# Performance work log

Measured on AMD Instinct MI355X. Metric: run time of the kernel, lower is better.

Reference implementation:

```python
import jax, jax.numpy as jnp
import numpy as np

B, T, IN, H, N, W, R, NW, OUT = 16, 64, 256, 512, 256, 64, 4, 1, 256
NM = 1 + 2 * NW  # read modes
EPS = 1e-6

# interface slice offsets
_sizes = [R*W, R, NW*W, NW, NW*W, NW*W, R, NW, NW, R*NM]
_offs = np.concatenate([[0], np.cumsum(_sizes)])

def _oneplus(x):
    return 1.0 + jax.nn.softplus(x)

def _content_weights(M, keys, strengths):
    # M: [B,N,W], keys: [B,h,W], strengths: [B,h] -> [B,h,N]
    Mn = M / (jnp.linalg.norm(M, axis=-1, keepdims=True) + EPS)
    kn = keys / (jnp.linalg.norm(keys, axis=-1, keepdims=True) + EPS)
    sim = jnp.einsum('bnw,bhw->bhn', Mn, kn)
    return jax.nn.softmax(_oneplus(strengths)[..., None] * sim, axis=-1)

def setup_inputs() -> dict:
    key = jax.random.key(0)
    ks = jax.random.split(key, 5)
    s = 0.02
    return {
        'inputs': jax.random.normal(ks[0], (T, B, IN), jnp.float32),
        'W_ih': jax.random.normal(ks[1], (4*H, IN + R*W), jnp.float32) * s,
        'W_hh': jax.random.normal(ks[2], (4*H, H), jnp.float32) * s,
        'b_ih': jnp.zeros((4*H,), jnp.float32),
        'b_hh': jnp.zeros((4*H,), jnp.float32),
        'W_int': jax.random.normal(ks[3], (H, int(_offs[-1])), jnp.float32) * s,
        'b_int': jnp.zeros((int(_offs[-1]),), jnp.float32),
        'W_out': jax.random.normal(ks[4], (OUT, H + R*W), jnp.float32) * s,
        'b_out': jnp.zeros((OUT,), jnp.float32),
    }

def _dnc_forward(inputs, W_ih, W_hh, b_ih, b_hh, W_int, b_int, W_out, b_out):
    off_diag = 1.0 - jnp.eye(N, dtype=inputs.dtype)

    def step(carry, x_t):
        h, c, M, usage, link, prec, wr, ww_prev, read_words = carry
        ctrl_in = jnp.concatenate([x_t, read_words.reshape(B, -1)], axis=1)
        gates = ctrl_in @ W_ih.T + h @ W_hh.T + (b_ih + b_hh)
        i, f, g, o = jnp.split(gates, 4, axis=1)  # torch LSTM gate order
        c = jax.nn.sigmoid(f) * c + jax.nn.sigmoid(i) * jnp.tanh(g)
        h = jax.nn.sigmoid(o) * jnp.tanh(c)

        itf = h @ W_int + b_int
        def sl(j, shape):
            return itf[:, _offs[j]:_offs[j+1]].reshape((B,) + shape)
        read_keys = sl(0, (R, W)); read_str = sl(1, (R,))
        write_keys = sl(2, (NW, W)); write_str = sl(3, (NW,))
        erase = jax.nn.sigmoid(sl(4, (NW, W)))
        write_vec = jax.nn.sigmoid(sl(5, (NW, W)))
        free_gate = jax.nn.sigmoid(sl(6, (R,)))
        alloc_gate = jax.nn.sigmoid(sl(7, (NW,)))
        write_gate = jax.nn.sigmoid(sl(8, (NW,)))
        modes = jax.nn.softmax(sl(9, (R, NM)), axis=2)

        # usage with previous write weights and free gates over previous reads
        psi = jnp.prod(1.0 - free_gate[:, :, None] * wr, axis=1)  # [B,N]
        ww_agg = 1.0 - jnp.prod(1.0 - ww_prev, axis=1)
        usage = (usage + ww_agg - usage * ww_agg) * psi

        # allocation weighting (sort ascending usage)
        idx = jnp.argsort(usage, axis=1)
        u_s = jnp.take_along_axis(usage, idx, axis=1)
        prod_excl = jnp.cumprod(jnp.concatenate([jnp.ones((B, 1), usage.dtype), u_s[:, :-1]], axis=1), axis=1)
        a_s = (1.0 - u_s) * prod_excl
        alloc = jnp.zeros_like(usage).at[jnp.arange(B)[:, None], idx].set(a_s)

        cw = _content_weights(M, write_keys, write_str)  # [B,NW,N]
        ww = write_gate[..., None] * (alloc_gate[..., None] * alloc[:, None, :] + (1.0 - alloc_gate[..., None]) * cw)

        # memory erase + write
        M = M * jnp.prod(1.0 - ww[:, :, :, None] * erase[:, :, None, :], axis=1)
        M = M + jnp.einsum('bhn,bhw->bnw', ww, write_vec)

        # temporal link update (uses old precedence)
        ww_i = ww[..., :, None]; ww_j = ww[..., None, :]
        link = (1.0 - ww_i - ww_j) * link + ww_i * prec[:, :, None, :]
        link = link * off_diag
        prec = (1.0 - ww.sum(-1, keepdims=True)) * prec + ww

        fwd = jnp.einsum('bwij,brj->brwi', link, wr)
        bwd = jnp.einsum('bwji,brj->brwi', link, wr)
        cr = _content_weights(M, read_keys, read_str)  # [B,R,N]
        mb, mf, mc = modes[..., :NW], modes[..., NW:2*NW], modes[..., 2*NW]
        wr = jnp.einsum('brw,brwn->brn', mb, bwd) + jnp.einsum('brw,brwn->brn', mf, fwd) + mc[..., None] * cr
        read_words = jnp.einsum('brn,bnw->brw', wr, M)

        pre = jnp.concatenate([h, read_words.reshape(B, -1)], axis=1)
        out = pre @ W_out.T + b_out
        return (h, c, M, usage, link, prec, wr, ww, read_words), out

    z = jnp.zeros
    dt = inputs.dtype
    carry0 = (z((B, H), dt), z((B, H), dt), z((B, N, W), dt), z((B, N), dt),
              z((B, NW, N, N), dt), z((B, NW, N), dt), z((B, R, N), dt),
              z((B, NW, N), dt), z((B, R, W), dt))
    _, outs = jax.lax.scan(step, carry0, inputs)
    return outs  # [T,B,OUT]

def reference(inputs, W_ih, W_hh, b_ih, b_hh, W_int, b_int, W_out, b_out):
    return _dnc_forward(inputs, W_ih, W_hh, b_ih, b_hh, W_int, b_int, W_out, b_out)
```

## Files before the change

### kernel.cpp

```cpp
#include <hip/hip_runtime.h>
#include <math.h>

#define BT 256
#define GRID 144

#define Bx 16
#define Tt 64
#define INx 256

__device__ __forceinline__ float sigm(float v) { return 1.0f / (1.0f + expf(-v)); }
__device__ __forceinline__ float oneplusf(float v) { return 1.0f + ((v > 15.0f) ? v : log1pf(expf(v))); }
__device__ __forceinline__ float4 ld4(const float* p) { return *reinterpret_cast<const float4*>(p); }

#define SCOPE_A __HIP_MEMORY_SCOPE_AGENT
__device__ __forceinline__ float gld(const float* p) {
    return __hip_atomic_load(p, __ATOMIC_RELAXED, SCOPE_A);
}
__device__ __forceinline__ void gst(float* p, float v) {
    __hip_atomic_store(p, v, __ATOMIC_RELAXED, SCOPE_A);
}
__device__ __forceinline__ float2 gld2(const float* p) {
    union { unsigned long long u; float2 f; } c;
    c.u = __hip_atomic_load(reinterpret_cast<const unsigned long long*>(p), __ATOMIC_RELAXED, SCOPE_A);
    return c.f;
}
__device__ __forceinline__ unsigned gldU(const unsigned* p) {
    return __hip_atomic_load(p, __ATOMIC_RELAXED, SCOPE_A);
}
__device__ __forceinline__ void gstU(unsigned* p, unsigned v) {
    __hip_atomic_store(p, v, __ATOMIC_RELAXED, SCOPE_A);
}

__device__ unsigned int g_flags[GRID];
__device__ unsigned int g_gen = 0;

__device__ __forceinline__ void gsync(unsigned tgt) {
    asm volatile("" ::: "memory");
    __builtin_amdgcn_s_waitcnt(0);
    __syncthreads();
    const int tid = threadIdx.x;
    if (blockIdx.x == 0) {
        if (tid < GRID) {
            if (tid == 0) gstU(&g_flags[0], tgt);
            while (gldU(&g_flags[tid]) < tgt) __builtin_amdgcn_s_sleep(1);
        }
        __syncthreads();
        if (tid == 0) gstU(&g_gen, tgt);
    } else {
        if (tid == 0) {
            gstU(&g_flags[blockIdx.x], tgt);
            while (gldU(&g_gen) < tgt) __builtin_amdgcn_s_sleep(1);
        }
        __syncthreads();
    }
    asm volatile("" ::: "memory");
}

#define ZERO_FLOATS 1376256

__global__ __launch_bounds__(BT)
void k_dnc(const float* __restrict__ x,
           const float* __restrict__ W_ih, const float* __restrict__ W_hh,
           const float* __restrict__ b_ih, const float* __restrict__ b_hh,
           const float* __restrict__ W_int, const float* __restrict__ b_int,
           const float* __restrict__ W_out, const float* __restrict__ b_out,
           float* __restrict__ outp, float* __restrict__ ws)
{
    const int bl = blockIdx.x, tid = threadIdx.x;

    float* h0   = ws;
    float* h1   = ws + 8192;
    float* cst  = ws + 16384;
    float* Mb   = ws + 24576;
    float* usg  = ws + 286720;
    float* lnk  = ws + 290816;
    float* pr0  = ws + 1339392;
    float* pr1  = ws + 1343488;
    float* wrb  = ws + 1347584;
    float* wwb  = ws + 1363968;
    float* rwb  = ws + 1368064;
    float* nrm  = ws + 1372160;
    float* itf  = ws + 1376256;
    float* ers  = ws + 1383792;
    float* wvs  = ws + 1384816;
    float* rso  = ws + 1385840;
    float* mds  = ws + 1385904;
    float* oh   = ws + 1386096;
    float* bwdb = ws + 1402480;
    float* fwdb = ws + 1418864;

    __shared__ float smem[4096];
    __shared__ int s_idx[256];
    __shared__ unsigned s_base;

    if (tid == 0) s_base = gldU(&g_gen);
    __syncthreads();
    unsigned bseq = s_base;

    for (int i = bl * BT + tid; i < ZERO_FLOATS; i += GRID * BT) gst(ws + i, 0.0f);
    gsync(++bseq);

    for (int t = 0; t < Tt; ++t) {
        const float* hr = (t & 1) ? h1 : h0;
        float*       hw = (t & 1) ? h0 : h1;
        const float* pr_r = (t & 1) ? pr1 : pr0;
        float*       pr_w = (t & 1) ? pr0 : pr1;

        if (bl < 128) {
            float* red = smem;
            int pl = tid >> 2, ks = tid & 3;
            int p = bl * 64 + pl;
            int b = p & 15, j = p >> 4;
            float a0 = 0, a1 = 0, a2 = 0, a3 = 0;
            const float *w0, *w1, *w2, *w3;
            int kofs = (ks < 2) ? ks * 256 : (ks - 2) * 256;
            if (ks < 2) {
                w0 = W_ih + (j)        * 512 + kofs;
                w1 = W_ih + (j + 512)  * 512 + kofs;
                w2 = W_ih + (j + 1024) * 512 + kofs;
                w3 = W_ih + (j + 1536) * 512 + kofs;
            } else {
                w0 = W_hh + (j)        * 512 + kofs;
                w1 = W_hh + (j + 512)  * 512 + kofs;
                w2 = W_hh + (j + 1024) * 512 + kofs;
                w3 = W_hh + (j + 1536) * 512 + kofs;
            }
            if (ks == 0) {
                const float* src = x + (t * Bx + b) * INx;
                for (int kk = 0; kk < 256; kk += 4) {
                    float4 iv = ld4(src + kk);
                    float4 q0 = ld4(w0 + kk);
                    a0 += iv.x * q0.x + iv.y * q0.y + iv.z * q0.z + iv.w * q0.w;
                    float4 q1 = ld4(w1 + kk);
                    a1 += iv.x * q1.x + iv.y * q1.y + iv.z * q1.z + iv.w * q1.w;
                    float4 q2 = ld4(w2 + kk);
                    a2 += iv.x * q2.x + iv.y * q2.y + iv.z * q2.z + iv.w * q2.w;
                    float4 q3 = ld4(w3 + kk);
                    a3 += iv.x * q3.x + iv.y * q3.y + iv.z * q3.z + iv.w * q3.w;
                }
            } else {
                const float* src = (ks == 1) ? (rwb + b * 256) : (hr + b * 512 + kofs);
                for (int kk = 0; kk < 256; kk += 4) {
                    float2 i0 = gld2(src + kk), i1 = gld2(src + kk + 2);
                    float4 q0 = ld4(w0 + kk);
                    a0 += i0.x * q0.x + i0.y * q0.y + i1.x * q0.z + i1.y * q0.w;
                    float4 q1 = ld4(w1 + kk);
                    a1 += i0.x * q1.x + i0.y * q1.y + i1.x * q1.z + i1.y * q1.w;
                    float4 q2 = ld4(w2 + kk);
                    a2 += i0.x * q2.x + i0.y * q2.y + i1.x * q2.z + i1.y * q2.w;
                    float4 q3 = ld4(w3 + kk);
                    a3 += i0.x * q3.x + i0.y * q3.y + i1.x * q3.z + i1.y * q3.w;
                }
            }
            red[pl * 16 + 0 * 4 + ks] = a0;
            red[pl * 16 + 1 * 4 + ks] = a1;
            red[pl * 16 + 2 * 4 + ks] = a2;
            red[pl * 16 + 3 * 4 + ks] = a3;
            __syncthreads();
            if (ks == 0) {
                const float* rp = red + pl * 16;
                float gi = rp[0]  + rp[1]  + rp[2]  + rp[3]  + b_ih[j]        + b_hh[j];
                float gf = rp[4]  + rp[5]  + rp[6]  + rp[7]  + b_ih[j + 512]  + b_hh[j + 512];
                float gg = rp[8]  + rp[9]  + rp[10] + rp[11] + b_ih[j + 1024] + b_hh[j + 1024];
                float go = rp[12] + rp[13] + rp[14] + rp[15] + b_ih[j + 1536] + b_hh[j + 1536];
                float cv = cst[b * 512 + j];
                cv = sigm(gf) * cv + sigm(gi) * tanhf(gg);
                float hv = sigm(go) * tanhf(cv);
                cst[b * 512 + j] = cv;
                gst(hw + b * 512 + j, hv);
            }
        } else if (t > 0) {
            int b = bl - 128, o = tid;
            float acc = b_out[o];
            acc += gld(oh + b * 256 + o) + gld(oh + (16 + b) * 256 + o)
                 + gld(oh + (32 + b) * 256 + o) + gld(oh + (48 + b) * 256 + o);
            const float* wrow = W_out + o * 768 + 512;
            const float* rwp = rwb + b * 256;
            for (int k = 0; k < 256; k += 4) {
                float4 w4 = ld4(wrow + k);
                float2 r0 = gld2(rwp + k), r1 = gld2(rwp + k + 2);
                acc += r0.x * w4.x + r0.y * w4.y + r1.x * w4.z + r1.y * w4.w;
            }
            outp[((t - 1) * Bx + b) * 256 + o] = acc;
        }
        gsync(++bseq);

        if (bl < 15) {
            int jl = tid & 31, ks = tid >> 5;
            int j = bl * 32 + jl;
            float acc[16];
#pragma unroll
            for (int b = 0; b < 16; b++) acc[b] = 0.f;
            for (int pass = 0; pass < 2; ++pass) {
                if (pass) __syncthreads();
                for (int m = tid; m < 2048; m += 256) {
                    int b = m >> 7, kk = (m & 127) << 1;
                    float2 v = gld2(hw + b * 512 + pass * 256 + kk);
                    smem[b * 256 + kk]     = v.x;
                    smem[b * 256 + kk + 1] = v.y;
                }
                __syncthreads();
                if (j < 471) {
                    for (int kk = ks * 32; kk < ks * 32 + 32; ++kk) {
                        float wv = W_int[(pass * 256 + kk) * 471 + j];
#pragma unroll
                        for (int b = 0; b < 16; b++) acc[b] += smem[b * 256 + kk] * wv;
                    }
                }
            }
            __syncthreads();
#pragma unroll
            for (int b = 0; b < 16; b++) smem[tid * 16 + b] = acc[b];
            __syncthreads();
            int jl2 = tid & 31, bh = tid >> 5;
            int j2 = bl * 32 + jl2;
            for (int rep = 0; rep < 2; ++rep) {
                int b2 = bh + 8 * rep;
                if (j2 < 471) {
                    float s = 0;
#pragma unroll
                    for (int ksx = 0; ksx < 8; ksx++) s += smem[(ksx * 32 + jl2) * 16 + b2];
                    gst(itf + b2 * 471 + j2, s + b_int[j2]);
                }
            }
        } else if (bl < 79) {
            int idx = bl - 15;
            int b = idx >> 2, ks = idx & 3;
            int o = tid;
            const float* wrow = W_out + o * 768 + ks * 128;
            const float* hb = hw + b * 512 + ks * 128;
            float acc = 0;
            for (int k = 0; k < 128; k += 4) {
                float4 w4 = ld4(wrow + k);
                float2 hA = gld2(hb + k), hB = gld2(hb + k + 2);
                acc += hA.x * w4.x + hA.y * w4.y + hB.x * w4.z + hB.y * w4.w;
            }
            gst(oh + (ks * 16 + b) * 256 + o, acc);
        }
        gsync(++bseq);

        if (bl < 16) {
            const int b = bl;
            float* s_keys = smem;
            float* s_cw   = smem + 256;
            float* s_al   = smem + 512;
            float* s_tmp  = smem + 768;
            float* s_wk   = smem + 1024;
            float* s_sc   = smem + 1088;
            const float* it = itf + b * 471;

            gst(bwdb + b * 1024 + tid, 0.f);
            gst(bwdb + b * 1024 + 256 + tid, 0.f);
            gst(bwdb + b * 1024 + 512 + tid, 0.f);
            gst(bwdb + b * 1024 + 768 + tid, 0.f);

            if (tid < 4) {
                float m0 = gld(it + 459 + tid * 3), m1 = gld(it + 460 + tid * 3), m2 = gld(it + 461 + tid * 3);
                float mx3 = fmaxf(m0, fmaxf(m1, m2));
                float e0 = expf(m0 - mx3), e1 = expf(m1 - mx3), e2 = expf(m2 - mx3);
                float inv = 1.f / (e0 + e1 + e2);
                gst(mds + (b * 4 + tid) * 3 + 0, e0 * inv);
                gst(mds + (b * 4 + tid) * 3 + 1, e1 * inv);
                gst(mds + (b * 4 + tid) * 3 + 2, e2 * inv);
                gst(rso + b * 4 + tid, oneplusf(gld(it + 256 + tid)));
                s_sc[tid] = sigm(gld(it + 453 + tid));
            }
            if (tid == 4) s_sc[4] = sigm(gld(it + 457));
            if (tid == 5) s_sc[5] = sigm(gld(it + 458));
            if (tid == 6) s_sc[6] = oneplusf(gld(it + 324));
            if (tid < 64) {
                gst(ers + b * 64 + tid, sigm(gld(it + 325 + tid)));
                gst(wvs + b * 64 + tid, sigm(gld(it + 389 + tid)));
                s_wk[tid] = gld(it + 260 + tid);
            }
            __syncthreads();
            if (tid < 64) {
                float v = s_wk[tid] * s_wk[tid];
                for (int o2 = 32; o2 > 0; o2 >>= 1) v += __shfl_down(v, o2);
                if (tid == 0) s_sc[7] = sqrtf(v);
            }
            __syncthreads();
            {
                int n = tid;
                float psi = 1.f;
#pragma unroll
                for (int r = 0; r < 4; r++) psi *= (1.f - s_sc[r] * gld(wrb + b * 1024 + r * 256 + n));
                float wwp = gld(wwb + b * 256 + n);
                float u = usg[b * 256 + n];
                u = (u + wwp - u * wwp) * psi;
                usg[b * 256 + n] = u;
                s_keys[n] = u;
                s_idx[n] = n;
                const float* Mr = Mb + (b * 256 + n) * 64;
                float dot = 0;
                for (int w = 0; w < 64; w += 2) {
                    float2 m2 = gld2(Mr + w);
                    dot += m2.x * s_wk[w] + m2.y * s_wk[w + 1];
                }
                s_cw[n] = s_sc[6] * dot / ((gld(nrm + b * 256 + n) + 1e-6f) * (s_sc[7] + 1e-6f));
            }
            __syncthreads();
            s_tmp[tid] = s_cw[tid];
            __syncthreads();
            for (int s2 = 128; s2 > 0; s2 >>= 1) { if (tid < s2) s_tmp[tid] = fmaxf(s_tmp[tid], s_tmp[tid + s2]); __syncthreads(); }
            float mx = s_tmp[0];
            __syncthreads();
            float ex = expf(s_cw[tid] - mx);
            s_tmp[tid] = ex;
            __syncthreads();
            for (int s2 = 128; s2 > 0; s2 >>= 1) { if (tid < s2) s_tmp[tid] += s_tmp[tid + s2]; __syncthreads(); }
            float cwv = ex / s_tmp[0];
            __syncthreads();
            s_cw[tid] = cwv;
            for (int kk2 = 2; kk2 <= 256; kk2 <<= 1) {
                for (int j2 = kk2 >> 1; j2 > 0; j2 >>= 1) {
                    int ixj = tid ^ j2;
                    if (ixj > tid) {
                        float ka = s_keys[tid], kb = s_keys[ixj];
                        int ia = s_idx[tid], ib = s_idx[ixj];
                        bool up = ((tid & kk2) == 0);
                        bool sw = up ? (kb < ka || (kb == ka && ib < ia))
                                     : (ka < kb || (ka == kb && ia < ib));
                        if (sw) { s_keys[tid] = kb; s_keys[ixj] = ka; s_idx[tid] = ib; s_idx[ixj] = ia; }
                    }
                    __syncthreads();
                }
            }
            s_tmp[tid] = s_keys[tid];
            __syncthreads();
            for (int o2 = 1; o2 < 256; o2 <<= 1) {
                float pv = (tid >= o2) ? s_tmp[tid - o2] : 1.0f;
                __syncthreads();
                s_tmp[tid] *= pv;
                __syncthreads();
            }
            float excl = (tid == 0) ? 1.0f : s_tmp[tid - 1];
            float a_s = (1.0f - s_keys[tid]) * excl;
            s_al[s_idx[tid]] = a_s;
            __syncthreads();
            float ag = s_sc[4], wg = s_sc[5];
            float wwn = wg * (ag * s_al[tid] + (1.f - ag) * s_cw[tid]);
            gst(wwb + b * 256 + tid, wwn);
            s_tmp[tid] = wwn;
            __syncthreads();
            for (int s2 = 128; s2 > 0; s2 >>= 1) { if (tid < s2) s_tmp[tid] += s_tmp[tid + s2]; __syncthreads(); }
            float S = s_tmp[0];
            gst(pr_w + b * 256 + tid, (1.f - S) * gld(pr_r + b * 256 + tid) + wwn);
        }
        gsync(++bseq);

        if (bl < 128) {
            int b = bl >> 3, ch = bl & 7;
            int ci = tid;
            float* s_wrL = smem;
            float* s_ww  = smem + 1024;
            float* s_fp  = smem + 1280;
            {
                float2 v0 = gld2(wrb + b * 1024 + tid * 4);
                float2 v1 = gld2(wrb + b * 1024 + tid * 4 + 2);
                s_wrL[tid * 4 + 0] = v0.x; s_wrL[tid * 4 + 1] = v0.y;
                s_wrL[tid * 4 + 2] = v1.x; s_wrL[tid * 4 + 3] = v1.y;
                s_ww[tid] = gld(wwb + b * 256 + tid);
            }
            __syncthreads();
            float wwc = s_ww[ci];
            float pco = gld(pr_r + b * 256 + ci);
            float* Lb = lnk + b * 65536;
            float b0 = 0, b1 = 0, b2 = 0, b3 = 0;
            int r0 = ch * 32;
            int wv = tid >> 6, lane = tid & 63;
            for (int rr = 0; rr < 32; ++rr) {
                int ri = r0 + rr;
                float wwr = s_ww[ri];
                float v = Lb[ri * 256 + ci];
                v = (1.f - wwr - wwc) * v + wwr * pco;
                if (ci == ri) v = 0.f;
                Lb[ri * 256 + ci] = v;
                b0 += v * s_wrL[ri];
                b1 += v * s_wrL[256 + ri];
                b2 += v * s_wrL[512 + ri];
                b3 += v * s_wrL[768 + ri];
                float p0 = v * s_wrL[ci];
                float p1 = v * s_wrL[256 + ci];
                float p2 = v * s_wrL[512 + ci];
                float p3 = v * s_wrL[768 + ci];
                for (int o2 = 32; o2 > 0; o2 >>= 1) {
                    p0 += __shfl_down(p0, o2); p1 += __shfl_down(p1, o2);
                    p2 += __shfl_down(p2, o2); p3 += __shfl_down(p3, o2);
                }
                if (lane == 0) {
                    s_fp[(rr * 4 + 0) * 4 + wv] = p0;
                    s_fp[(rr * 4 + 1) * 4 + wv] = p1;
                    s_fp[(rr * 4 + 2) * 4 + wv] = p2;
                    s_fp[(rr * 4 + 3) * 4 + wv] = p3;
                }
            }
            __syncthreads();
            if (tid < 128) {
                int rr = tid >> 2, r = tid & 3;
                const float* fp = s_fp + (rr * 4 + r) * 4;
                gst(fwdb + b * 1024 + r * 256 + (r0 + rr), fp[0] + fp[1] + fp[2] + fp[3]);
            }
            atomicAdd(bwdb + b * 1024 + ci, b0);
            atomicAdd(bwdb + b * 1024 + 256 + ci, b1);
            atomicAdd(bwdb + b * 1024 + 512 + ci, b2);
            atomicAdd(bwdb + b * 1024 + 768 + ci, b3);
        } else {
            int b = bl - 128;
            float* s_ww = smem;
            s_ww[tid] = gld(wwb + b * 256 + tid);
            __syncthreads();
            int w = tid & 63, rg = tid >> 6;
            float er = gld(ers + b * 64 + w), wv = gld(wvs + b * 64 + w);
            for (int it2 = 0; it2 < 64; ++it2) {
                int n = rg + 4 * it2;
                float wwn = s_ww[n];
                float m = gld(Mb + (b * 256 + n) * 64 + w);
                m = m * (1.f - wwn * er) + wwn * wv;
                gst(Mb + (b * 256 + n) * 64 + w, m);
                float s = m * m;
                for (int o2 = 32; o2 > 0; o2 >>= 1) s += __shfl_down(s, o2);
                if (w == 0) gst(nrm + b * 256 + n, sqrtf(s));
            }
        }
        gsync(++bseq);

        if (bl < 64) {
            int b = bl >> 2, r = bl & 3;
            float* s_wr  = smem;
            float* s_tmp = smem + 512;
            float* s_key = smem + 768;
            float* s_sc  = smem + 840;
            s_wr[tid] = gld(wrb + b * 1024 + r * 256 + tid);
            if (tid < 64) s_key[tid] = gld(itf + b * 471 + r * 64 + tid);
            __syncthreads();
            if (tid < 64) {
                float v = s_key[tid] * s_key[tid];
                for (int o2 = 32; o2 > 0; o2 >>= 1) v += __shfl_down(v, o2);
                if (tid == 0) s_sc[0] = sqrtf(v);
            }
            __syncthreads();
            int n = tid;
            float bwd_n = gld(bwdb + b * 1024 + r * 256 + n);
            float fwd_n = gld(fwdb + b * 1024 + r * 256 + n);
            const float* Mr = Mb + (b * 256 + n) * 64;
            float dot = 0;
            for (int w = 0; w < 64; w += 2) {
                float2 m2 = gld2(Mr + w);
                dot += m2.x * s_key[w] + m2.y * s_key[w + 1];
            }
            float simv = gld(rso + b * 4 + r) * dot / ((gld(nrm + b * 256 + n) + 1e-6f) * (s_sc[0] + 1e-6f));
            s_tmp[tid] = simv;
            __syncthreads();
            for (int s2 = 128; s2 > 0; s2 >>= 1) { if (tid < s2) s_tmp[tid] = fmaxf(s_tmp[tid], s_tmp[tid + s2]); __syncthreads(); }
            float mx = s_tmp[0];
            __syncthreads();
            float ex = expf(simv - mx);
            s_tmp[tid] = ex;
            __syncthreads();
            for (int s2 = 128; s2 > 0; s2 >>= 1) { if (tid < s2) s_tmp[tid] += s_tmp[tid + s2]; __syncthreads(); }
            float crv = ex / s_tmp[0];
            float mbv = gld(mds + (b * 4 + r) * 3 + 0);
            float mfv = gld(mds + (b * 4 + r) * 3 + 1);
            float mcv = gld(mds + (b * 4 + r) * 3 + 2);
            float wrn = mbv * bwd_n + mfv * fwd_n + mcv * crv;
            gst(wrb + b * 1024 + r * 256 + n, wrn);
            __syncthreads();
            s_wr[tid] = wrn;
            __syncthreads();
            int w = tid & 63, gq = tid >> 6;
            float p = 0;
            const float* Mg = Mb + b * 256 * 64;
            for (int n2 = gq * 64; n2 < gq * 64 + 64; ++n2)
                p += s_wr[n2] * gld(Mg + n2 * 64 + w);
            s_tmp[tid] = p;
            __syncthreads();
            if (tid < 64)
                gst(rwb + b * 256 + r * 64 + tid,
                    s_tmp[tid] + s_tmp[tid + 64] + s_tmp[tid + 128] + s_tmp[tid + 192]);
        }
        gsync(++bseq);
    }

    if (bl < 16) {
        int b = bl, o = tid;
        float acc = b_out[o];
        acc += gld(oh + b * 256 + o) + gld(oh + (16 + b) * 256 + o)
             + gld(oh + (32 + b) * 256 + o) + gld(oh + (48 + b) * 256 + o);
        const float* wrow = W_out + o * 768 + 512;
        const float* rwp = rwb + b * 256;
        for (int k = 0; k < 256; k += 4) {
            float4 w4 = ld4(wrow + k);
            float2 r0 = gld2(rwp + k), r1 = gld2(rwp + k + 2);
            acc += r0.x * w4.x + r0.y * w4.y + r1.x * w4.z + r1.y * w4.w;
        }
        outp[((Tt - 1) * Bx + b) * 256 + o] = acc;
    }
}

extern "C" void kernel_launch(void* const* d_in, const int* in_sizes, int n_in,
                              void* d_out, int out_size, void* d_ws, size_t ws_size,
                              hipStream_t stream) {
    const float* x     = (const float*)d_in[0];
    const float* W_ih  = (const float*)d_in[1];
    const float* W_hh  = (const float*)d_in[2];
    const float* b_ih  = (const float*)d_in[3];
    const float* b_hh  = (const float*)d_in[4];
    const float* W_int = (const float*)d_in[5];
    const float* b_int = (const float*)d_in[6];
    const float* W_out = (const float*)d_in[7];
    const float* b_out = (const float*)d_in[8];
    float* outp = (float*)d_out;
    float* ws   = (float*)d_ws;

    k_dnc<<<GRID, BT, 0, stream>>>(x, W_ih, W_hh, b_ih, b_hh, W_int, b_int,
                                   W_out, b_out, outp, ws);
}
```

Measured before the change: 10.06 ms.

## Stage activations and memory matrix in shared memory across DNC phases

```diff
diff --git a/kernel.cpp b/kernel.cpp
--- a/kernel.cpp
+++ b/kernel.cpp
@@ -6,11 +6,11 @@
 
 #define Bx 16
 #define Tt 64
-#define INx 256
 
 __device__ __forceinline__ float sigm(float v) { return 1.0f / (1.0f + expf(-v)); }
 __device__ __forceinline__ float oneplusf(float v) { return 1.0f + ((v > 15.0f) ? v : log1pf(expf(v))); }
 __device__ __forceinline__ float4 ld4(const float* p) { return *reinterpret_cast<const float4*>(p); }
+__device__ __forceinline__ float2 ld2f(const float* p) { return *reinterpret_cast<const float2*>(p); }
 
 #define SCOPE_A __HIP_MEMORY_SCOPE_AGENT
 __device__ __forceinline__ float gld(const float* p) {
@@ -23,6 +23,11 @@
     union { unsigned long long u; float2 f; } c;
     c.u = __hip_atomic_load(reinterpret_cast<const unsigned long long*>(p), __ATOMIC_RELAXED, SCOPE_A);
     return c.f;
+}
+__device__ __forceinline__ void gst2(float* p, float a, float b2) {
+    union { unsigned long long u; float2 f; } c;
+    c.f.x = a; c.f.y = b2;
+    __hip_atomic_store(reinterpret_cast<unsigned long long*>(p), c.u, __ATOMIC_RELAXED, SCOPE_A);
 }
 __device__ __forceinline__ unsigned gldU(const unsigned* p) {
     return __hip_atomic_load(p, __ATOMIC_RELAXED, SCOPE_A);
@@ -89,7 +94,8 @@
     float* bwdb = ws + 1402480;
     float* fwdb = ws + 1418864;
 
-    __shared__ float smem[4096];
+    __shared__ __align__(16) float sbig[16576];
+    __shared__ __align__(16) float smem[4096];
     __shared__ int s_idx[256];
     __shared__ unsigned s_base;
 
@@ -107,11 +113,29 @@
         float*       pr_w = (t & 1) ? pr0 : pr1;
 
         if (bl < 128) {
+            {
+                const float* xb = x + (size_t)t * (Bx * 256);
+                for (int i = tid; i < 2048; i += BT) {
+                    int b2 = i >> 7, q = (i & 127) * 2;
+                    float2 v = ld2f(xb + b2 * 256 + q);
+                    *reinterpret_cast<float2*>(&sbig[b2 * 260 + q]) = v;
+                }
+                for (int i = tid; i < 2048; i += BT) {
+                    int b2 = i >> 7, q = (i & 127) * 2;
+                    float2 v = gld2(rwb + b2 * 256 + q);
+                    *reinterpret_cast<float2*>(&sbig[4160 + b2 * 260 + q]) = v;
+                }
+                for (int i = tid; i < 4096; i += BT) {
+                    int b2 = i >> 8, q = (i & 255) * 2;
+                    float2 v = gld2(hr + b2 * 512 + q);
+                    *reinterpret_cast<float2*>(&sbig[8320 + b2 * 516 + q]) = v;
+                }
+            }
+            __syncthreads();
             float* red = smem;
             int pl = tid >> 2, ks = tid & 3;
             int p = bl * 64 + pl;
             int b = p & 15, j = p >> 4;
-            float a0 = 0, a1 = 0, a2 = 0, a3 = 0;
             const float *w0, *w1, *w2, *w3;
             int kofs = (ks < 2) ? ks * 256 : (ks - 2) * 256;
             if (ks < 2) {
@@ -125,33 +149,22 @@
                 w2 = W_hh + (j + 1024) * 512 + kofs;
                 w3 = W_hh + (j + 1536) * 512 + kofs;
             }
-            if (ks == 0) {
-                const float* src = x + (t * Bx + b) * INx;
-                for (int kk = 0; kk < 256; kk += 4) {
-                    float4 iv = ld4(src + kk);
-                    float4 q0 = ld4(w0 + kk);
-                    a0 += iv.x * q0.x + iv.y * q0.y + iv.z * q0.z + iv.w * q0.w;
-                    float4 q1 = ld4(w1 + kk);
-                    a1 += iv.x * q1.x + iv.y * q1.y + iv.z * q1.z + iv.w * q1.w;
-                    float4 q2 = ld4(w2 + kk);
-                    a2 += iv.x * q2.x + iv.y * q2.y + iv.z * q2.z + iv.w * q2.w;
-                    float4 q3 = ld4(w3 + kk);
-                    a3 += iv.x * q3.x + iv.y * q3.y + iv.z * q3.z + iv.w * q3.w;
-                }
-            } else {
-                const float* src = (ks == 1) ? (rwb + b * 256) : (hr + b * 512 + kofs);
-                for (int kk = 0; kk < 256; kk += 4) {
-                    float2 i0 = gld2(src + kk), i1 = gld2(src + kk + 2);
-                    float4 q0 = ld4(w0 + kk);
-                    a0 += i0.x * q0.x + i0.y * q0.y + i1.x * q0.z + i1.y * q0.w;
-                    float4 q1 = ld4(w1 + kk);
-                    a1 += i0.x * q1.x + i0.y * q1.y + i1.x * q1.z + i1.y * q1.w;
-                    float4 q2 = ld4(w2 + kk);
-                    a2 += i0.x * q2.x + i0.y * q2.y + i1.x * q2.z + i1.y * q2.w;
-                    float4 q3 = ld4(w3 + kk);
-                    a3 += i0.x * q3.x + i0.y * q3.y + i1.x * q3.z + i1.y * q3.w;
-                }
-            }
+            const float* s = (ks == 0) ? &sbig[b * 260]
+                           : (ks == 1) ? &sbig[4160 + b * 260]
+                           :             &sbig[8320 + b * 516 + (ks - 2) * 256];
+            float a0 = 0, a1 = 0, a2 = 0, a3 = 0;
+            for (int kk = 0; kk < 256; kk += 4) {
+                float4 iv = *reinterpret_cast<const float4*>(s + kk);
+                float4 q0 = ld4(w0 + kk);
+                a0 += iv.x * q0.x + iv.y * q0.y + iv.z * q0.z + iv.w * q0.w;
+                float4 q1 = ld4(w1 + kk);
+                a1 += iv.x * q1.x + iv.y * q1.y + iv.z * q1.z + iv.w * q1.w;
+                float4 q2 = ld4(w2 + kk);
+                a2 += iv.x * q2.x + iv.y * q2.y + iv.z * q2.z + iv.w * q2.w;
+                float4 q3 = ld4(w3 + kk);
+                a3 += iv.x * q3.x + iv.y * q3.y + iv.z * q3.z + iv.w * q3.w;
+            }
+            __syncthreads();
             red[pl * 16 + 0 * 4 + ks] = a0;
             red[pl * 16 + 1 * 4 + ks] = a1;
             red[pl * 16 + 2 * 4 + ks] = a2;
@@ -170,42 +183,43 @@
                 gst(hw + b * 512 + j, hv);
             }
         } else if (t > 0) {
-            int b = bl - 128, o = tid;
+            int b = bl - 128;
+            if (tid < 128) {
+                float2 v = gld2(rwb + b * 256 + tid * 2);
+                *reinterpret_cast<float2*>(&smem[tid * 2]) = v;
+            }
+            __syncthreads();
+            int o = tid;
             float acc = b_out[o];
             acc += gld(oh + b * 256 + o) + gld(oh + (16 + b) * 256 + o)
                  + gld(oh + (32 + b) * 256 + o) + gld(oh + (48 + b) * 256 + o);
             const float* wrow = W_out + o * 768 + 512;
-            const float* rwp = rwb + b * 256;
             for (int k = 0; k < 256; k += 4) {
                 float4 w4 = ld4(wrow + k);
-                float2 r0 = gld2(rwp + k), r1 = gld2(rwp + k + 2);
-                acc += r0.x * w4.x + r0.y * w4.y + r1.x * w4.z + r1.y * w4.w;
-            }
-            outp[((t - 1) * Bx + b) * 256 + o] = acc;
+                float4 s4 = *reinterpret_cast<const float4*>(&smem[k]);
+                acc += s4.x * w4.x + s4.y * w4.y + s4.z * w4.z + s4.w * w4.w;
+            }
+            outp[((size_t)(t - 1) * Bx + b) * 256 + o] = acc;
         }
         gsync(++bseq);
 
         if (bl < 15) {
-            int jl = tid & 31, ks = tid >> 5;
+            for (int i = tid; i < 4096; i += BT) {
+                int b2 = i >> 8, q = (i & 255) * 2;
+                float2 v = gld2(hw + b2 * 512 + q);
+                *reinterpret_cast<float2*>(&sbig[b2 * 512 + q]) = v;
+            }
+            __syncthreads();
+            int jl = tid & 31, k8 = tid >> 5;
             int j = bl * 32 + jl;
             float acc[16];
 #pragma unroll
             for (int b = 0; b < 16; b++) acc[b] = 0.f;
-            for (int pass = 0; pass < 2; ++pass) {
-                if (pass) __syncthreads();
-                for (int m = tid; m < 2048; m += 256) {
-                    int b = m >> 7, kk = (m & 127) << 1;
-                    float2 v = gld2(hw + b * 512 + pass * 256 + kk);
-                    smem[b * 256 + kk]     = v.x;
-                    smem[b * 256 + kk + 1] = v.y;
-                }
-                __syncthreads();
-                if (j < 471) {
-                    for (int kk = ks * 32; kk < ks * 32 + 32; ++kk) {
-                        float wv = W_int[(pass * 256 + kk) * 471 + j];
+            if (j < 471) {
+                for (int k = k8 * 64; k < k8 * 64 + 64; ++k) {
+                    float wv = W_int[k * 471 + j];
 #pragma unroll
-                        for (int b = 0; b < 16; b++) acc[b] += smem[b * 256 + kk] * wv;
-                    }
+                    for (int b = 0; b < 16; b++) acc[b] += sbig[b * 512 + k] * wv;
                 }
             }
             __syncthreads();
@@ -226,14 +240,18 @@
         } else if (bl < 79) {
             int idx = bl - 15;
             int b = idx >> 2, ks = idx & 3;
+            if (tid < 64) {
+                float2 v = gld2(hw + b * 512 + ks * 128 + tid * 2);
+                *reinterpret_cast<float2*>(&smem[tid * 2]) = v;
+            }
+            __syncthreads();
             int o = tid;
             const float* wrow = W_out + o * 768 + ks * 128;
-            const float* hb = hw + b * 512 + ks * 128;
             float acc = 0;
             for (int k = 0; k < 128; k += 4) {
                 float4 w4 = ld4(wrow + k);
-                float2 hA = gld2(hb + k), hB = gld2(hb + k + 2);
-                acc += hA.x * w4.x + hA.y * w4.y + hB.x * w4.z + hB.y * w4.w;
+                float4 s4 = *reinterpret_cast<const float4*>(&smem[k]);
+                acc += s4.x * w4.x + s4.y * w4.y + s4.z * w4.z + s4.w * w4.w;
             }
             gst(oh + (ks * 16 + b) * 256 + o, acc);
         }
@@ -241,6 +259,12 @@
 
         if (bl < 16) {
             const int b = bl;
+            for (int i = tid; i < 8192; i += BT) {
+                int n = i >> 5, w2 = (i & 31) * 2;
+                float2 v = gld2(Mb + (b * 256 + n) * 64 + w2);
+                sbig[w2 * 256 + ((n + w2) & 255)] = v.x;
+                sbig[(w2 + 1) * 256 + ((n + w2 + 1) & 255)] = v.y;
+            }
             float* s_keys = smem;
             float* s_cw   = smem + 256;
             float* s_al   = smem + 512;
@@ -289,14 +313,10 @@
                 float u = usg[b * 256 + n];
                 u = (u + wwp - u * wwp) * psi;
                 usg[b * 256 + n] = u;
-                s_keys[n] = u;
-                s_idx[n] = n;
-                const float* Mr = Mb + (b * 256 + n) * 64;
-                float dot = 0;
-                for (int w = 0; w < 64; w += 2) {
-                    float2 m2 = gld2(Mr + w);
-                    dot += m2.x * s_wk[w] + m2.y * s_wk[w + 1];
-                }
+                s_keys[n] = u; s_idx[n] = n;
+                float dot = 0.f;
+                for (int w = 0; w < 64; ++w)
+                    dot += sbig[w * 256 + ((n + w) & 255)] * s_wk[w];
                 s_cw[n] = s_sc[6] * dot / ((gld(nrm + b * 256 + n) + 1e-6f) * (s_sc[7] + 1e-6f));
             }
             __syncthreads();
@@ -407,26 +427,42 @@
             atomicAdd(bwdb + b * 1024 + 768 + ci, b3);
         } else {
             int b = bl - 128;
-            float* s_ww = smem;
-            s_ww[tid] = gld(wwb + b * 256 + tid);
-            __syncthreads();
-            int w = tid & 63, rg = tid >> 6;
-            float er = gld(ers + b * 64 + w), wv = gld(wvs + b * 64 + w);
-            for (int it2 = 0; it2 < 64; ++it2) {
-                int n = rg + 4 * it2;
-                float wwn = s_ww[n];
-                float m = gld(Mb + (b * 256 + n) * 64 + w);
-                m = m * (1.f - wwn * er) + wwn * wv;
-                gst(Mb + (b * 256 + n) * 64 + w, m);
-                float s = m * m;
-                for (int o2 = 32; o2 > 0; o2 >>= 1) s += __shfl_down(s, o2);
-                if (w == 0) gst(nrm + b * 256 + n, sqrtf(s));
+            if (tid < 32) {
+                float2 v = gld2(ers + b * 64 + tid * 2);
+                *reinterpret_cast<float2*>(&smem[tid * 2]) = v;
+            } else if (tid < 64) {
+                int q = tid - 32;
+                float2 v = gld2(wvs + b * 64 + q * 2);
+                *reinterpret_cast<float2*>(&smem[64 + q * 2]) = v;
+            } else if (tid < 192) {
+                int q = tid - 64;
+                float2 v = gld2(wwb + b * 256 + q * 2);
+                *reinterpret_cast<float2*>(&smem[128 + q * 2]) = v;
+            }
+            __syncthreads();
+            int w2g = (tid & 31) * 2, ng = tid >> 5;
+            for (int i = 0; i < 32; ++i) {
+                int n = ng * 32 + i;
+                float wwn = smem[128 + n];
+                float2 m = gld2(Mb + (b * 256 + n) * 64 + w2g);
+                m.x = m.x * (1.f - wwn * smem[w2g])     + wwn * smem[64 + w2g];
+                m.y = m.y * (1.f - wwn * smem[w2g + 1]) + wwn * smem[64 + w2g + 1];
+                gst2(Mb + (b * 256 + n) * 64 + w2g, m.x, m.y);
+                float s = m.x * m.x + m.y * m.y;
+                for (int o2 = 16; o2 > 0; o2 >>= 1) s += __shfl_down(s, o2, 32);
+                if (w2g == 0) gst(nrm + b * 256 + n, sqrtf(s));
             }
         }
         gsync(++bseq);
 
         if (bl < 64) {
             int b = bl >> 2, r = bl & 3;
+            for (int i = tid; i < 8192; i += BT) {
+                int n = i >> 5, w2 = (i & 31) * 2;
+                float2 v = gld2(Mb + (b * 256 + n) * 64 + w2);
+                sbig[w2 * 256 + ((n + w2) & 255)] = v.x;
+                sbig[(w2 + 1) * 256 + ((n + w2 + 1) & 255)] = v.y;
+            }
             float* s_wr  = smem;
             float* s_tmp = smem + 512;
             float* s_key = smem + 768;
@@ -443,12 +479,9 @@
             int n = tid;
             float bwd_n = gld(bwdb + b * 1024 + r * 256 + n);
             float fwd_n = gld(fwdb + b * 1024 + r * 256 + n);
-            const float* Mr = Mb + (b * 256 + n) * 64;
-            float dot = 0;
-            for (int w = 0; w < 64; w += 2) {
-                float2 m2 = gld2(Mr + w);
-                dot += m2.x * s_key[w] + m2.y * s_key[w + 1];
-            }
+            float dot = 0.f;
+            for (int w = 0; w < 64; ++w)
+                dot += sbig[w * 256 + ((n + w) & 255)] * s_key[w];
             float simv = gld(rso + b * 4 + r) * dot / ((gld(nrm + b * 256 + n) + 1e-6f) * (s_sc[0] + 1e-6f));
             s_tmp[tid] = simv;
             __syncthreads();
@@ -469,11 +502,12 @@
             s_wr[tid] = wrn;
             __syncthreads();
             int w = tid & 63, gq = tid >> 6;
-            float p = 0;
-            const float* Mg = Mb + b * 256 * 64;
-            for (int n2 = gq * 64; n2 < gq * 64 + 64; ++n2)
-                p += s_wr[n2] * gld(Mg + n2 * 64 + w);
-            s_tmp[tid] = p;
+            float pacc = 0.f;
+            for (int k = 0; k < 64; ++k) {
+                int n2 = gq * 64 + k;
+                pacc += s_wr[n2] * sbig[w * 256 + ((n2 + w) & 255)];
+            }
+            s_tmp[tid] = pacc;
             __syncthreads();
             if (tid < 64)
                 gst(rwb + b * 256 + r * 64 + tid,
@@ -483,18 +517,23 @@
     }
 
     if (bl < 16) {
-        int b = bl, o = tid;
+        int b = bl;
+        if (tid < 128) {
+            float2 v = gld2(rwb + b * 256 + tid * 2);
+            *reinterpret_cast<float2*>(&smem[tid * 2]) = v;
+        }
+        __syncthreads();
+        int o = tid;
         float acc = b_out[o];
         acc += gld(oh + b * 256 + o) + gld(oh + (16 + b) * 256 + o)
              + gld(oh + (32 + b) * 256 + o) + gld(oh + (48 + b) * 256 + o);
         const float* wrow = W_out + o * 768 + 512;
-        const float* rwp = rwb + b * 256;
         for (int k = 0; k < 256; k += 4) {
             float4 w4 = ld4(wrow + k);
-            float2 r0 = gld2(rwp + k), r1 = gld2(rwp + k + 2);
-            acc += r0.x * w4.x + r0.y * w4.y + r1.x * w4.z + r1.y * w4.w;
-        }
-        outp[((Tt - 1) * Bx + b) * 256 + o] = acc;
+            float4 s4 = *reinterpret_cast<const float4*>(&smem[k]);
+            acc += s4.x * w4.x + s4.y * w4.y + s4.z * w4.z + s4.w * w4.w;
+        }
+        outp[((size_t)(Tt - 1) * Bx + b) * 256 + o] = acc;
     }
 }
 
@@ -512,6 +551,7 @@
     const float* b_out = (const float*)d_in[8];
     float* outp = (float*)d_out;
     float* ws   = (float*)d_ws;
+    (void)in_sizes; (void)n_in; (void)out_size; (void)ws_size;
 
     k_dnc<<<GRID, BT, 0, stream>>>(x, W_ih, W_hh, b_ih, b_hh, W_int, b_int,
                                    W_out, b_out, outp, ws);
```

Result: faster. 9.051 ms (-10.0%).
